# Kernel tuning notes

Hardware: AMD Instinct MI355X
Metric: run time of the kernel (lower is better)

The kernel has to match this reference:

```python
import jax, jax.numpy as jnp
import numpy as np

B, L, H = 2, 4096, 1024


def _rope_tables(seq_len, dim, base=10000.0):
    # standard RoPE cos/sin tables, rotate-half convention, shape [L, dim]
    inv_freq = 1.0 / (base ** (np.arange(0, dim, 2, dtype=np.float32) / dim))
    t = np.arange(seq_len, dtype=np.float32)
    freqs = np.outer(t, inv_freq)                      # [L, dim/2]
    emb = np.concatenate([freqs, freqs], axis=-1)      # [L, dim]
    return jnp.asarray(np.cos(emb)), jnp.asarray(np.sin(emb))


def setup_inputs() -> dict:
    key = jax.random.key(0)
    k1, k2 = jax.random.split(key)
    hidden_states = jax.random.normal(k1, (B, L, H), dtype=jnp.float32)
    # queries weight: normal with std = initializer_range / sqrt(2*num_layers*hidden)
    std = 0.02 / np.sqrt(2.0 * 24 * H)
    W_q = jax.random.normal(k2, (H, H), dtype=jnp.float32) * std
    cos, sin = _rope_tables(L, H)
    return {"hidden_states": hidden_states, "W_q": W_q, "cos": cos, "sin": sin}


def _rotate_half(x):
    x1, x2 = jnp.split(x, 2, axis=-1)
    return jnp.concatenate([-x2, x1], axis=-1)


def reference(hidden_states, W_q, cos, sin):
    # dropout with p=0.0 (eval) -> identity
    h = hidden_states * cos[None, :, :] + _rotate_half(hidden_states) * sin[None, :, :]  # RoPE, [B,L,H]
    q = jnp.einsum('blh,oh->blo', h, W_q)          # F.linear(h, W_q), [B,L,H]
    pre_attn = jnp.einsum('blh,bmh->blm', q, h)    # Q @ K^T (no softmax), [B,L,L]
    attention = jnp.einsum('blm,bmh->blh', pre_attn, h)  # scores @ V, [B,L,H]
    return attention
```

## Files before the change

### kernel.cpp

```cpp
#include <hip/hip_runtime.h>
#include <hip/hip_bf16.h>
#include <stdint.h>

#define BB 2
#define LL 4096
#define HH 1024
#define GBK 32

typedef __bf16 bf16;
typedef __bf16 bf16x4 __attribute__((ext_vector_type(4)));
typedef __bf16 bf16x8 __attribute__((ext_vector_type(8)));
typedef float  f32x4  __attribute__((ext_vector_type(4)));

__device__ __forceinline__ void async_cp16(const bf16* g, const bf16* l)
{
    typedef const uint32_t __attribute__((address_space(1)))* gp_t;
    typedef uint32_t __attribute__((address_space(3)))* lp_t;
    __builtin_amdgcn_global_load_lds((gp_t)(uintptr_t)g, (lp_t)(uintptr_t)l, 16, 0, 0);
}

__device__ __forceinline__ uint32_t pack_bf16(float lo, float hi)
{
    union { bf16 b; unsigned short u; } a, c;
    a.b = (bf16)lo; c.b = (bf16)hi;
    return (uint32_t)a.u | ((uint32_t)c.u << 16);
}

__global__ __launch_bounds__(256) void prep_kernel(
    const float* __restrict__ x, const float* __restrict__ cs,
    const float* __restrict__ sn, const float* __restrict__ Wq,
    bf16* __restrict__ h, bf16* __restrict__ hT, bf16* __restrict__ Wb)
{
    const int id = blockIdx.x;
    if (id >= 512) {
        const long base = (long)(id - 512) * 4096 + (long)threadIdx.x * 16;
#pragma unroll
        for (int j = 0; j < 4; ++j) {
            const float4 v = *(const float4*)(Wq + base + j * 4);
            bf16x4 o;
            o[0] = (bf16)v.x; o[1] = (bf16)v.y; o[2] = (bf16)v.z; o[3] = (bf16)v.w;
            *(bf16x4*)(Wb + base + j * 4) = o;
        }
        return;
    }
    __shared__ uint32_t lds[2][64][36];
    const int r0 = (id >> 3) * 64;
    const int c0 = (id & 7) * 64;
    const int t  = threadIdx.x;
    const int c8 = t & 7;
    const int rr = t >> 3;
    const int ca = c0 + c8 * 8;
    const long crow0 = (long)(r0 + 2 * rr) * HH;

    float cA[2][8], sA[2][8];
#pragma unroll
    for (int rw = 0; rw < 2; ++rw) {
        const long cr = crow0 + (long)rw * HH;
        *(float4*)&cA[rw][0] = *(const float4*)(cs + cr + ca);
        *(float4*)&cA[rw][4] = *(const float4*)(cs + cr + ca + 4);
        *(float4*)&sA[rw][0] = *(const float4*)(sn + cr + ca);
        *(float4*)&sA[rw][4] = *(const float4*)(sn + cr + ca + 4);
    }

    for (int b = 0; b < 2; ++b) {
        if (b) __syncthreads();
        float oA[2][8], oB[2][8];
#pragma unroll
        for (int rw = 0; rw < 2; ++rw) {
            const long xr = ((long)b * LL + r0 + 2 * rr + rw) * HH;
            float xA[8], xB[8];
            *(float4*)&xA[0] = *(const float4*)(x + xr + ca);
            *(float4*)&xA[4] = *(const float4*)(x + xr + ca + 4);
            *(float4*)&xB[0] = *(const float4*)(x + xr + ca + 512);
            *(float4*)&xB[4] = *(const float4*)(x + xr + ca + 516);
#pragma unroll
            for (int j = 0; j < 8; ++j) {
                oA[rw][j] = xA[j] * cA[rw][j] - xB[j] * sA[rw][j];
                oB[rw][j] = xB[j] * cA[rw][j] + xA[j] * sA[rw][j];
            }
            bf16x8 hA, hB;
#pragma unroll
            for (int j = 0; j < 8; ++j) { hA[j] = (bf16)oA[rw][j]; hB[j] = (bf16)oB[rw][j]; }
            *(bf16x8*)(h + xr + ca)       = hA;
            *(bf16x8*)(h + xr + ca + 512) = hB;
        }
#pragma unroll
        for (int j = 0; j < 8; ++j) {
            lds[0][c8 * 8 + j][rr] = pack_bf16(oA[0][j], oA[1][j]);
            lds[1][c8 * 8 + j][rr] = pack_bf16(oB[0][j], oB[1][j]);
        }
        __syncthreads();

        const int cc = t >> 2;
        const int q  = t & 3;
#pragma unroll
        for (int s = 0; s < 2; ++s) {
            const int hrow = (s ? c0 + 512 : c0) + cc;
            bf16* po = hT + (long)b * HH * LL + (long)hrow * LL + r0 + q * 16;
            const uint4 w0 = *(const uint4*)&lds[s][cc][q * 8];
            const uint4 w1 = *(const uint4*)&lds[s][cc][q * 8 + 4];
            *(uint4*)(po)     = w0;
            *(uint4*)(po + 8) = w1;
        }
    }
}

__global__ __launch_bounds__(128) void rope_kernel(
    const float* __restrict__ x, const float* __restrict__ cs,
    const float* __restrict__ sn, bf16* __restrict__ h)
{
    const int l = blockIdx.x;
    const int b = blockIdx.y;
    const int i = threadIdx.x * 4;
    const long xb = ((long)b * LL + l) * HH;
    const long cb = (long)l * HH;
    const float4 x1 = *(const float4*)(x + xb + i);
    const float4 x2 = *(const float4*)(x + xb + i + HH / 2);
    const float4 c1 = *(const float4*)(cs + cb + i);
    const float4 c2 = *(const float4*)(cs + cb + i + HH / 2);
    const float4 s1 = *(const float4*)(sn + cb + i);
    const float4 s2 = *(const float4*)(sn + cb + i + HH / 2);
    bf16x4 o1, o2;
    o1[0] = (bf16)(x1.x * c1.x - x2.x * s1.x);
    o1[1] = (bf16)(x1.y * c1.y - x2.y * s1.y);
    o1[2] = (bf16)(x1.z * c1.z - x2.z * s1.z);
    o1[3] = (bf16)(x1.w * c1.w - x2.w * s1.w);
    o2[0] = (bf16)(x2.x * c2.x + x1.x * s2.x);
    o2[1] = (bf16)(x2.y * c2.y + x1.y * s2.y);
    o2[2] = (bf16)(x2.z * c2.z + x1.z * s2.z);
    o2[3] = (bf16)(x2.w * c2.w + x1.w * s2.w);
    *(bf16x4*)(h + xb + i)          = o1;
    *(bf16x4*)(h + xb + i + HH / 2) = o2;
}

__global__ __launch_bounds__(256) void transpose_bf16_64(
    const bf16* __restrict__ in, bf16* __restrict__ out, const int R, const int C)
{
    __shared__ uint32_t lds[64][36];
    const long zoff = (long)blockIdx.z * R * C;
    const int r0 = blockIdx.x * 64;
    const int c0 = blockIdx.y * 64;
    const int t  = threadIdx.x;
    const int c8 = t & 7;
    const int rr = t >> 3;
    const bf16* p0 = in + zoff + (long)(r0 + 2 * rr) * C + c0 + c8 * 8;
    const uint4 ra = *(const uint4*)p0;
    const uint4 rb = *(const uint4*)(p0 + C);
    const uint32_t av[4] = {ra.x, ra.y, ra.z, ra.w};
    const uint32_t bv[4] = {rb.x, rb.y, rb.z, rb.w};
#pragma unroll
    for (int j = 0; j < 4; ++j) {
        const uint32_t alo = av[j] & 0xffffu, ahi = av[j] >> 16;
        const uint32_t blo = bv[j] & 0xffffu, bhi = bv[j] >> 16;
        lds[c8 * 8 + 2 * j    ][rr] = alo | (blo << 16);
        lds[c8 * 8 + 2 * j + 1][rr] = ahi | (bhi << 16);
    }
    __syncthreads();
    const int c = t >> 2;
    const int q = t & 3;
    const uint4 w0 = *(const uint4*)&lds[c][q * 8];
    const uint4 w1 = *(const uint4*)&lds[c][q * 8 + 4];
    bf16* po = out + zoff + (long)(c0 + c) * R + r0 + q * 16;
    *(uint4*)(po)     = w0;
    *(uint4*)(po + 8) = w1;
}

__global__ __launch_bounds__(256) void cast_wq(
    const float* __restrict__ Wq, bf16* __restrict__ Wb)
{
    const long idx = ((long)blockIdx.x * 256 + threadIdx.x) * 4;
    const float4 v = *(const float4*)(Wq + idx);
    bf16x4 o;
    o[0] = (bf16)v.x; o[1] = (bf16)v.y; o[2] = (bf16)v.z; o[3] = (bf16)v.w;
    *(bf16x4*)(Wb + idx) = o;
}

#define GEMM_SHARED()                                                          \
    __shared__ __align__(16) bf16 As_[2][128][32];                             \
    __shared__ __align__(16) bf16 Bs_[2][128][32];

#define GEMM_PREFETCH(KOFF, BUF)                                               \
    do {                                                                       \
        async_cp16(Ag + (KOFF),           &As_[BUF][0][0] + woff0);            \
        async_cp16(Ag + (KOFF) + 64L * K, &As_[BUF][0][0] + woff1);            \
        async_cp16(Bg + (KOFF),           &Bs_[BUF][0][0] + woff0);            \
        async_cp16(Bg + (KOFF) + 64L * K, &Bs_[BUF][0][0] + woff1);            \
    } while (0)

#define GEMM_BODY(M0, N0, KBASE, KEND, DST, DT, LDN)                           \
    {                                                                          \
        const int tid  = threadIdx.x;                                          \
        const int lane = tid & 63;                                             \
        const int wave = tid >> 6;                                             \
        const int wm = (wave & 1) * 64;                                        \
        const int wn = (wave >> 1) * 64;                                       \
        const int fr = lane & 15;                                              \
        const int fq = lane >> 4;                                              \
        const int srow = tid >> 2;                                             \
        const int scol = (tid & 3) * 8;                                        \
        const int woff0 = wave * 512;                                          \
        const int woff1 = 2048 + wave * 512;                                   \
        const bf16* Ag = Ab + (long)((M0) + srow) * K + scol;                  \
        const bf16* Bg = Bb + (long)((N0) + srow) * K + scol;                  \
        const f32x4 vzero = {0.f, 0.f, 0.f, 0.f};                              \
        f32x4 acc[4][4];                                                       \
        _Pragma("unroll") for (int i = 0; i < 4; ++i)                          \
            _Pragma("unroll") for (int j = 0; j < 4; ++j) acc[i][j] = vzero;   \
        GEMM_PREFETCH(KBASE, 0);                                               \
        int buf = 0;                                                           \
        for (int k0 = (KBASE); k0 < (KEND); k0 += GBK, buf ^= 1) {             \
            __syncthreads();                                                   \
            if (k0 + GBK < (KEND)) GEMM_PREFETCH(k0 + GBK, buf ^ 1);           \
            bf16x8 af[4], bfv[4];                                              \
            _Pragma("unroll") for (int i = 0; i < 4; ++i)                      \
                af[i]  = *(const bf16x8*)&As_[buf][wm + i * 16 + fr][fq * 8];  \
            _Pragma("unroll") for (int j = 0; j < 4; ++j)                      \
                bfv[j] = *(const bf16x8*)&Bs_[buf][wn + j * 16 + fr][fq * 8];  \
            _Pragma("unroll") for (int i = 0; i < 4; ++i)                      \
                _Pragma("unroll") for (int j = 0; j < 4; ++j)                  \
                    acc[i][j] = __builtin_amdgcn_mfma_f32_16x16x32_bf16(       \
                        af[i], bfv[j], acc[i][j], 0, 0, 0);                    \
        }                                                                      \
        _Pragma("unroll") for (int i = 0; i < 4; ++i) {                        \
            _Pragma("unroll") for (int r = 0; r < 4; ++r) {                    \
                const int row = (M0) + wm + i * 16 + fq * 4 + r;               \
                _Pragma("unroll") for (int j = 0; j < 4; ++j) {                \
                    const int col = (N0) + wn + j * 16 + fr;                   \
                    (DST)[(long)row * (LDN) + col] = (DT)acc[i][j][r];         \
                }                                                              \
            }                                                                  \
        }                                                                      \
    }

template <typename OUT_T>
__global__ __launch_bounds__(256) void gemm_bt(
    const bf16* __restrict__ A, const bf16* __restrict__ B, OUT_T* __restrict__ C,
    const int M, const int N, const int K,
    const long sA, const long sB, const long sC)
{
    GEMM_SHARED();
    const bf16* Ab = A + blockIdx.z * sA;
    const bf16* Bb = B + blockIdx.z * sB;
    OUT_T*      Cb = C + blockIdx.z * sC;
    const int m0 = blockIdx.x * 128;
    const int n0 = blockIdx.y * 128;
    GEMM_BODY(m0, n0, 0, K, Cb, OUT_T, N);
}

#define E_STAGE_A(KT, PART, BUF)                                               \
  do {                                                                         \
    const int kk0_ = kbase + (KT) * 64;                                        \
    _Pragma("unroll") for (int qq_ = 0; qq_ < 2; ++qq_) {                      \
      const int ch_  = qq_ * 512 + tid;                                        \
      const int sl_  = ch_ >> 3;                                               \
      const int cc_  = (ch_ & 7) ^ (sl_ & 7);                                  \
      const int row_ = (sl_ & 63) + (PART) * 64 + ((sl_ >> 6) << 7);           \
      async_cp16(Ab + (long)(m0 + row_) * K + kk0_ + cc_ * 8,                  \
                 &As[BUF][PART][0][0] + (qq_ * 512 + (tid & 448)) * 8);        \
    }                                                                          \
  } while (0)

#define E_STAGE_B(KT, PART, BUF)                                               \
  do {                                                                         \
    const int kk0_ = kbase + (KT) * 64;                                        \
    _Pragma("unroll") for (int qq_ = 0; qq_ < 2; ++qq_) {                      \
      const int ch_  = qq_ * 512 + tid;                                        \
      const int sl_  = ch_ >> 3;                                               \
      const int cc_  = (ch_ & 7) ^ (sl_ & 7);                                  \
      const int row_ = (sl_ & 31) + (PART) * 32 + ((sl_ >> 5) << 6);           \
      async_cp16(Bb + (long)(n0 + row_) * K + kk0_ + cc_ * 8,                  \
                 &Bs[BUF][PART][0][0] + (qq_ * 512 + (tid & 448)) * 8);        \
    }                                                                          \
  } while (0)

#define E_STAGE_B2(KT, PART, BUF)                                              \
  do {                                                                         \
    const int kk0_ = kbase + (KT) * 64;                                        \
    const int sl_  = tid >> 3;                                                 \
    const int cc_  = (tid & 7) ^ (sl_ & 7);                                    \
    const int row_ = (sl_ & 15) + (PART) * 16 + ((sl_ >> 4) << 5);             \
    async_cp16(Bb + (long)(n0 + row_) * K + kk0_ + cc_ * 8,                    \
               &Bs2[BUF][PART][0][0] + (tid & 448) * 8);                       \
  } while (0)

#define E_LOAD_A(BUF, IG)                                                      \
  do {                                                                         \
    const bf16* Ap_ = &As[BUF][IG][0][0] + (wr * 64 + fr) * 64;                \
    _Pragma("unroll") for (int ii_ = 0; ii_ < 4; ++ii_)                        \
      _Pragma("unroll") for (int kk_ = 0; kk_ < 2; ++kk_)                      \
        af[ii_][kk_] = *(const bf16x8*)(Ap_ + ii_ * 1024 +                     \
                        (((kk_ * 4 + fq) ^ fr7) * 8));                         \
  } while (0)

#define E_LOAD_Bv(BUF, JP, DSTV)                                               \
  do {                                                                         \
    const bf16* Bp_ = &Bs[BUF][JP][0][0] + (wc * 32 + fr) * 64;                \
    _Pragma("unroll") for (int jj_ = 0; jj_ < 2; ++jj_)                        \
      _Pragma("unroll") for (int kk_ = 0; kk_ < 2; ++kk_)                      \
        DSTV[jj_][kk_] = *(const bf16x8*)(Bp_ + jj_ * 1024 +                   \
                        (((kk_ * 4 + fq) ^ fr7) * 8));                         \
  } while (0)

#define E_LOAD_B2(BUF, JG, DSTV)                                               \
  do {                                                                         \
    const bf16* Bp_ = &Bs2[BUF][JG][0][0] + (wc * 16 + fr) * 64;               \
    _Pragma("unroll") for (int kk_ = 0; kk_ < 2; ++kk_)                        \
      DSTV[kk_] = *(const bf16x8*)(Bp_ + (((kk_ * 4 + fq) ^ fr7) * 8));        \
  } while (0)

#define E_MMA(IG, JG, BV)                                                      \
  do {                                                                         \
    __builtin_amdgcn_s_setprio(1);                                             \
    _Pragma("unroll") for (int ii_ = 0; ii_ < 4; ++ii_)                        \
      _Pragma("unroll") for (int jj_ = 0; jj_ < 2; ++jj_)                      \
        _Pragma("unroll") for (int kk_ = 0; kk_ < 2; ++kk_)                    \
          acc[(IG) * 4 + ii_][(JG) * 2 + jj_] =                                \
              __builtin_amdgcn_mfma_f32_16x16x32_bf16(                         \
                  af[ii_][kk_], BV[jj_][kk_],                                  \
                  acc[(IG) * 4 + ii_][(JG) * 2 + jj_], 0, 0, 0);               \
    __builtin_amdgcn_s_setprio(0);                                             \
  } while (0)

#define E_MMA2(IG, JG, BV)                                                     \
  do {                                                                         \
    __builtin_amdgcn_s_setprio(1);                                             \
    _Pragma("unroll") for (int ii_ = 0; ii_ < 4; ++ii_)                        \
      _Pragma("unroll") for (int kk_ = 0; kk_ < 2; ++kk_)                      \
        acc2[(IG) * 4 + ii_][JG] =                                             \
            __builtin_amdgcn_mfma_f32_16x16x32_bf16(                           \
                af[ii_][kk_], BV[kk_], acc2[(IG) * 4 + ii_][JG], 0, 0, 0);     \
    __builtin_amdgcn_s_setprio(0);                                             \
  } while (0)

#define E_BAR()   __builtin_amdgcn_s_barrier()
#define E_LGKM0() do { asm volatile("s_waitcnt lgkmcnt(0)" ::: "memory");      \
                       __builtin_amdgcn_sched_barrier(0); } while (0)
#define E_VM(N)   asm volatile("s_waitcnt vmcnt(" #N ")" ::: "memory")

#define E_COMMON_IDX()                                                         \
  const int tid  = threadIdx.x;                                                \
  const int lane = tid & 63;                                                   \
  const int wv   = tid >> 6;                                                   \
  const int wr   = wv >> 2;                                                    \
  const int wc   = wv & 3;                                                     \
  const int fr   = lane & 15;                                                  \
  const int fq   = lane >> 4;                                                  \
  const int fr7  = fr & 7;                                                     \
  (void)lane;

__global__ __launch_bounds__(512, 2) void gemm8_Gq(
    const bf16* __restrict__ hT, const bf16* __restrict__ Wb,
    const bf16* __restrict__ h, bf16* __restrict__ P, bf16* __restrict__ q)
{
    __shared__ __align__(16) bf16 As[2][2][128][64];
    __shared__ __align__(16) bf16 Bs[2][2][128][64];
    E_COMMON_IDX();
    bf16x8 af[4][2], bfv0[2][2], bfv1[2][2];
    f32x4 acc[8][4];
#pragma unroll
    for (int i_ = 0; i_ < 8; ++i_)
#pragma unroll
        for (int j_ = 0; j_ < 4; ++j_) acc[i_][j_] = (f32x4){0.f, 0.f, 0.f, 0.f};

    const int bid = blockIdx.x;
    const int id  = (bid & 7) * 32 + (bid >> 3);
    const bf16* Ab; const bf16* Bb;
    int K, kbase, m0, n0;
    bf16* Cb;
    if (id < 128) {
        m0 = (id >> 2) * 256;
        n0 = (id & 3) * 256;
        Ab = h; Bb = Wb; K = HH; kbase = 0;
        Cb = q;
    } else {
        const int u  = id - 128;
        const int pl = u >> 4;
        const int zb = pl >> 2;
        const int zs = pl & 3;
        const int tl = u & 15;
        m0 = (tl & 3) * 256;
        n0 = (tl >> 2) * 256;
        Ab = hT + (long)zb * HH * LL; Bb = Ab;
        K  = LL; kbase = zs * (LL / 4);
        Cb = P + (long)pl * HH * HH;
    }

    E_STAGE_A(0, 0, 0); E_STAGE_B(0, 1, 0); E_STAGE_A(0, 1, 0);
    E_STAGE_B(0, 0, 0);
    E_STAGE_A(1, 0, 1); E_STAGE_B(1, 1, 1); E_STAGE_A(1, 1, 1);
    E_VM(6); E_BAR();
    int t_ = 0;
#pragma unroll 1
    for (; t_ + 3 < 16; t_ += 2) {
         E_LOAD_A(0, 0); E_LOAD_Bv(0, 0, bfv0); E_STAGE_B(t_ + 1, 0, 1);
                 E_BAR(); E_LGKM0(); E_MMA(0, 0, bfv0); E_BAR();
         E_LOAD_Bv(0, 1, bfv1); E_STAGE_A(t_ + 2, 0, 0);
                 E_BAR(); E_LGKM0(); E_MMA(0, 1, bfv1); E_BAR();
         E_LOAD_A(0, 1); E_STAGE_B(t_ + 2, 1, 0);
                 E_BAR(); E_LGKM0(); E_MMA(1, 1, bfv1); E_BAR();
         E_STAGE_A(t_ + 2, 1, 0);
                 E_MMA(1, 0, bfv0); E_VM(6); E_BAR();
         E_LOAD_A(1, 0); E_LOAD_Bv(1, 0, bfv0); E_STAGE_B(t_ + 2, 0, 0);
                 E_BAR(); E_LGKM0(); E_MMA(0, 0, bfv0); E_BAR();
         E_LOAD_Bv(1, 1, bfv1); E_STAGE_A(t_ + 3, 0, 1);
                 E_BAR(); E_LGKM0(); E_MMA(0, 1, bfv1); E_BAR();
         E_LOAD_A(1, 1); E_STAGE_B(t_ + 3, 1, 1);
                 E_BAR(); E_LGKM0(); E_MMA(1, 1, bfv1); E_BAR();
         E_STAGE_A(t_ + 3, 1, 1);
                 E_MMA(1, 0, bfv0); E_VM(6); E_BAR();
    }
    E_LOAD_A(0, 0); E_LOAD_Bv(0, 0, bfv0); E_STAGE_B(t_ + 1, 0, 1);
    E_BAR(); E_LGKM0(); E_MMA(0, 0, bfv0); E_BAR();
    E_LOAD_Bv(0, 1, bfv1); E_BAR(); E_LGKM0(); E_MMA(0, 1, bfv1); E_BAR();
    E_LOAD_A(0, 1); E_BAR(); E_LGKM0(); E_MMA(1, 1, bfv1); E_BAR();
    E_MMA(1, 0, bfv0); E_VM(0); E_BAR();
    E_LOAD_A(1, 0); E_LOAD_Bv(1, 0, bfv0); E_BAR(); E_LGKM0(); E_MMA(0, 0, bfv0); E_BAR();
    E_LOAD_Bv(1, 1, bfv1); E_BAR(); E_LGKM0(); E_MMA(0, 1, bfv1); E_BAR();
    E_LOAD_A(1, 1); E_BAR(); E_LGKM0(); E_MMA(1, 1, bfv1); E_BAR();
    E_MMA(1, 0, bfv0);

#pragma unroll
    for (int gi = 0; gi < 8; ++gi)
#pragma unroll
        for (int r = 0; r < 4; ++r) {
            const int row = m0 + wr * 128 + gi * 16 + fq * 4 + r;
#pragma unroll
            for (int gj = 0; gj < 4; ++gj)
                Cb[(long)row * HH + n0 + wc * 64 + gj * 16 + fr] = (bf16)acc[gi][gj][r];
        }
}

__global__ __launch_bounds__(512, 2) void gemm8_qG(
    const bf16* __restrict__ qm, const bf16* __restrict__ G, float* __restrict__ out)
{
    __shared__ __align__(16) bf16 As[2][2][128][64];
    __shared__ __align__(16) bf16 Bs2[2][2][64][64];
    E_COMMON_IDX();
    bf16x8 af[4][2], bw0[2], bw1[2];
    f32x4 acc2[8][2];
#pragma unroll
    for (int i_ = 0; i_ < 8; ++i_)
#pragma unroll
        for (int j_ = 0; j_ < 2; ++j_) acc2[i_][j_] = (f32x4){0.f, 0.f, 0.f, 0.f};

    const int bid = blockIdx.x;
    const int id  = (bid & 7) * 32 + (bid >> 3);
    const int mb  = id >> 3;
    const int b   = mb >> 4;
    const int m0  = (mb & 15) * 256;
    const int n0  = (id & 7) * 128;
    const bf16* Ab = qm + (long)b * LL * HH;
    const bf16* Bb = G + (long)b * HH * HH;
    const int K = HH, kbase = 0;
    float* outb = out + (long)b * LL * HH;

    E_STAGE_A(0, 0, 0); E_STAGE_B2(0, 1, 0); E_STAGE_A(0, 1, 0);
    E_STAGE_B2(0, 0, 0);
    E_STAGE_A(1, 0, 1); E_STAGE_B2(1, 1, 1); E_STAGE_A(1, 1, 1);
    E_VM(5); E_BAR();
    int t_ = 0;
#pragma unroll 1
    for (; t_ + 3 < 16; t_ += 2) {
         E_LOAD_A(0, 0); E_LOAD_B2(0, 0, bw0); E_STAGE_B2(t_ + 1, 0, 1);
                 E_BAR(); E_LGKM0(); E_MMA2(0, 0, bw0); E_BAR();
         E_LOAD_B2(0, 1, bw1); E_STAGE_A(t_ + 2, 0, 0);
                 E_BAR(); E_LGKM0(); E_MMA2(0, 1, bw1); E_BAR();
         E_LOAD_A(0, 1); E_STAGE_B2(t_ + 2, 1, 0);
                 E_BAR(); E_LGKM0(); E_MMA2(1, 1, bw1); E_BAR();
         E_STAGE_A(t_ + 2, 1, 0);
                 E_MMA2(1, 0, bw0); E_VM(5); E_BAR();
         E_LOAD_A(1, 0); E_LOAD_B2(1, 0, bw0); E_STAGE_B2(t_ + 2, 0, 0);
                 E_BAR(); E_LGKM0(); E_MMA2(0, 0, bw0); E_BAR();
         E_LOAD_B2(1, 1, bw1); E_STAGE_A(t_ + 3, 0, 1);
                 E_BAR(); E_LGKM0(); E_MMA2(0, 1, bw1); E_BAR();
         E_LOAD_A(1, 1); E_STAGE_B2(t_ + 3, 1, 1);
                 E_BAR(); E_LGKM0(); E_MMA2(1, 1, bw1); E_BAR();
         E_STAGE_A(t_ + 3, 1, 1);
                 E_MMA2(1, 0, bw0); E_VM(5); E_BAR();
    }
    E_LOAD_A(0, 0); E_LOAD_B2(0, 0, bw0); E_STAGE_B2(t_ + 1, 0, 1);
    E_BAR(); E_LGKM0(); E_MMA2(0, 0, bw0); E_BAR();
    E_LOAD_B2(0, 1, bw1); E_BAR(); E_LGKM0(); E_MMA2(0, 1, bw1); E_BAR();
    E_LOAD_A(0, 1); E_BAR(); E_LGKM0(); E_MMA2(1, 1, bw1); E_BAR();
    E_MMA2(1, 0, bw0); E_VM(0); E_BAR();
    E_LOAD_A(1, 0); E_LOAD_B2(1, 0, bw0); E_BAR(); E_LGKM0(); E_MMA2(0, 0, bw0); E_BAR();
    E_LOAD_B2(1, 1, bw1); E_BAR(); E_LGKM0(); E_MMA2(0, 1, bw1); E_BAR();
    E_LOAD_A(1, 1); E_BAR(); E_LGKM0(); E_MMA2(1, 1, bw1); E_BAR();
    E_MMA2(1, 0, bw0);

#pragma unroll
    for (int gi = 0; gi < 8; ++gi)
#pragma unroll
        for (int r = 0; r < 4; ++r) {
            const int row = m0 + wr * 128 + gi * 16 + fq * 4 + r;
#pragma unroll
            for (int gj = 0; gj < 2; ++gj)
                outb[(long)row * HH + n0 + wc * 32 + gj * 16 + fr] = acc2[gi][gj][r];
        }
}

__global__ __launch_bounds__(256) void reduce_splits(
    const bf16* __restrict__ P, bf16* __restrict__ out, const int npb, const int S)
{
    const int b = blockIdx.y;
    const long r = ((long)blockIdx.x * 256 + threadIdx.x) * 8;
    const bf16* base = P + (long)b * S * npb + r;
    float a[8];
    {
        const bf16x8 v = *(const bf16x8*)(base);
#pragma unroll
        for (int j = 0; j < 8; ++j) a[j] = (float)v[j];
    }
    for (int s = 1; s < S; ++s) {
        const bf16x8 v = *(const bf16x8*)(base + (long)s * npb);
#pragma unroll
        for (int j = 0; j < 8; ++j) a[j] += (float)v[j];
    }
    bf16x8 o;
#pragma unroll
    for (int j = 0; j < 8; ++j) o[j] = (bf16)a[j];
    *(bf16x8*)(out + (long)b * npb + r) = o;
}

extern "C" void kernel_launch(void* const* d_in, const int* in_sizes, int n_in,
                              void* d_out, int out_size, void* d_ws, size_t ws_size,
                              hipStream_t stream)
{
    const float* x  = (const float*)d_in[0];
    const float* Wq = (const float*)d_in[1];
    const float* cs = (const float*)d_in[2];
    const float* sn = (const float*)d_in[3];
    float* out = (float*)d_out;
    char* ws = (char*)d_ws;

    bf16*  h  = (bf16*)(ws);
    bf16*  hT = (bf16*)(ws + 16u * 1024 * 1024);
    bf16*  Wb = (bf16*)(ws + 32u * 1024 * 1024);
    bf16*  G  = (bf16*)(ws + 34u * 1024 * 1024);
    bf16*  P  = (bf16*)(ws + 38u * 1024 * 1024);

    const bool big_ws = ws_size >= (size_t)90 * 1024 * 1024;
    bf16* q = big_ws ? (bf16*)(ws + 70u * 1024 * 1024)
                     : (bf16*)(ws + 54u * 1024 * 1024);

    if (big_ws) {
        prep_kernel<<<dim3(768), 256, 0, stream>>>(x, cs, sn, Wq, h, hT, Wb);
        gemm8_Gq<<<dim3(256), 512, 0, stream>>>(hT, Wb, h, P, q);
        reduce_splits<<<dim3(HH * HH / 2048, BB), 256, 0, stream>>>(P, G, HH * HH, 4);
        gemm8_qG<<<dim3(256), 512, 0, stream>>>(q, G, out);
    } else {
        rope_kernel<<<dim3(LL, BB), 128, 0, stream>>>(x, cs, sn, h);
        transpose_bf16_64<<<dim3(LL / 64, HH / 64, BB), 256, 0, stream>>>(h, hT, LL, HH);
        cast_wq<<<dim3(HH * HH / 1024), 256, 0, stream>>>(Wq, Wb);
        gemm_bt<bf16><<<dim3(HH / 128, HH / 128, BB), 256, 0, stream>>>(
            hT, hT, G, HH, HH, LL, (long)HH * LL, (long)HH * LL, (long)HH * HH);
        gemm_bt<bf16><<<dim3(LL / 128, HH / 128, BB), 256, 0, stream>>>(
            h, Wb, q, LL, HH, HH, (long)LL * HH, 0L, (long)LL * HH);
        gemm_bt<float><<<dim3(LL / 128, HH / 128, BB), 256, 0, stream>>>(
            q, G, out, LL, HH, HH, (long)LL * HH, (long)HH * HH, (long)LL * HH);
    }
}
```

Baseline: 167.7 us.

## Reassociate matmuls to form Wq·G once instead of projecting all queries

Exploits associativity: the per-token query projection q = h·Wqᵀ is no longer computed. Instead a small per-batch 1024×1024 matrix M = G·Wq is formed and used directly as the right-hand operand of the final GEMM (out = h·Mᵀ, relying on G being symmetric). This cuts the large L×H×H projection GEMM and replaces it with an H×H×H split-K GEMM plus an extra reduction. The prep kernel now transposes Wq while casting it, and the G GEMM is re-split into 8 K-chunks so it still fills 256 blocks. The cost is two extra kernel launches on the critical path and an extra bf16 rounding of M.

```diff
diff --git a/kernel.cpp b/kernel.cpp
--- a/kernel.cpp
+++ b/kernel.cpp
@@ -29,24 +29,39 @@
 __global__ __launch_bounds__(256) void prep_kernel(
     const float* __restrict__ x, const float* __restrict__ cs,
     const float* __restrict__ sn, const float* __restrict__ Wq,
-    bf16* __restrict__ h, bf16* __restrict__ hT, bf16* __restrict__ Wb)
+    bf16* __restrict__ h, bf16* __restrict__ hT, bf16* __restrict__ WqT)
 {
     const int id = blockIdx.x;
+    const int t  = threadIdx.x;
     if (id >= 512) {
-        const long base = (long)(id - 512) * 4096 + (long)threadIdx.x * 16;
-#pragma unroll
-        for (int j = 0; j < 4; ++j) {
-            const float4 v = *(const float4*)(Wq + base + j * 4);
-            bf16x4 o;
-            o[0] = (bf16)v.x; o[1] = (bf16)v.y; o[2] = (bf16)v.z; o[3] = (bf16)v.w;
-            *(bf16x4*)(Wb + base + j * 4) = o;
-        }
+        __shared__ uint32_t tl[64][36];
+        const int id2 = id - 512;
+        const int tr0 = (id2 >> 4) * 64;
+        const int tc0 = (id2 & 15) * 64;
+        const int c8 = t & 7;
+        const int rr = t >> 3;
+        const float* p0 = Wq + (long)(tr0 + 2 * rr) * HH + tc0 + c8 * 8;
+        float ra[8], rb[8];
+        *(float4*)&ra[0] = *(const float4*)(p0);
+        *(float4*)&ra[4] = *(const float4*)(p0 + 4);
+        *(float4*)&rb[0] = *(const float4*)(p0 + HH);
+        *(float4*)&rb[4] = *(const float4*)(p0 + HH + 4);
+#pragma unroll
+        for (int j = 0; j < 8; ++j)
+            tl[c8 * 8 + j][rr] = pack_bf16(ra[j], rb[j]);
+        __syncthreads();
+        const int cc = t >> 2;
+        const int qq = t & 3;
+        bf16* po = WqT + (long)(tc0 + cc) * HH + tr0 + qq * 16;
+        const uint4 w0 = *(const uint4*)&tl[cc][qq * 8];
+        const uint4 w1 = *(const uint4*)&tl[cc][qq * 8 + 4];
+        *(uint4*)(po)     = w0;
+        *(uint4*)(po + 8) = w1;
         return;
     }
     __shared__ uint32_t lds[2][64][36];
     const int r0 = (id >> 3) * 64;
     const int c0 = (id & 7) * 64;
-    const int t  = threadIdx.x;
     const int c8 = t & 7;
     const int rr = t >> 3;
     const int ca = c0 + c8 * 8;
@@ -247,6 +262,25 @@
     GEMM_BODY(m0, n0, 0, K, Cb, OUT_T, N);
 }
 
+__global__ __launch_bounds__(256) void gemm_mt(
+    const bf16* __restrict__ G, const bf16* __restrict__ WqT, bf16* __restrict__ Pm)
+{
+    GEMM_SHARED();
+    const int id = blockIdx.x;
+    const int b  = id >> 8;
+    const int rs = id & 255;
+    const int s  = rs >> 6;
+    const int tl = rs & 63;
+    const int m0 = (tl & 7) * 128;
+    const int n0 = (tl >> 3) * 128;
+    const bf16* Ab = G + (long)b * HH * HH;
+    const bf16* Bb = WqT;
+    bf16* Cb = Pm + (long)(b * 4 + s) * HH * HH;
+    const int K = HH;
+    const int kbase = s * 256;
+    GEMM_BODY(m0, n0, kbase, kbase + 256, Cb, bf16, HH);
+}
+
 #define E_STAGE_A(KT, PART, BUF)                                               \
   do {                                                                         \
     const int kk0_ = kbase + (KT) * 64;                                        \
@@ -348,9 +382,8 @@
   const int fr7  = fr & 7;                                                     \
   (void)lane;
 
-__global__ __launch_bounds__(512, 2) void gemm8_Gq(
-    const bf16* __restrict__ hT, const bf16* __restrict__ Wb,
-    const bf16* __restrict__ h, bf16* __restrict__ P, bf16* __restrict__ q)
+__global__ __launch_bounds__(512, 2) void gemm8_G(
+    const bf16* __restrict__ hT, bf16* __restrict__ P)
 {
     __shared__ __align__(16) bf16 As[2][2][128][64];
     __shared__ __align__(16) bf16 Bs[2][2][128][64];
@@ -364,26 +397,17 @@
 
     const int bid = blockIdx.x;
     const int id  = (bid & 7) * 32 + (bid >> 3);
-    const bf16* Ab; const bf16* Bb;
-    int K, kbase, m0, n0;
-    bf16* Cb;
-    if (id < 128) {
-        m0 = (id >> 2) * 256;
-        n0 = (id & 3) * 256;
-        Ab = h; Bb = Wb; K = HH; kbase = 0;
-        Cb = q;
-    } else {
-        const int u  = id - 128;
-        const int pl = u >> 4;
-        const int zb = pl >> 2;
-        const int zs = pl & 3;
-        const int tl = u & 15;
-        m0 = (tl & 3) * 256;
-        n0 = (tl >> 2) * 256;
-        Ab = hT + (long)zb * HH * LL; Bb = Ab;
-        K  = LL; kbase = zs * (LL / 4);
-        Cb = P + (long)pl * HH * HH;
-    }
+    const int pl  = id >> 4;
+    const int zb  = pl >> 3;
+    const int zs  = pl & 7;
+    const int tl  = id & 15;
+    const int m0  = (tl & 3) * 256;
+    const int n0  = (tl >> 2) * 256;
+    const bf16* Ab = hT + (long)zb * HH * LL;
+    const bf16* Bb = Ab;
+    const int K = LL;
+    const int kbase = zs * (LL / 8);
+    bf16* Cb = P + (long)pl * HH * HH;
 
     E_STAGE_A(0, 0, 0); E_STAGE_B(0, 1, 0); E_STAGE_A(0, 1, 0);
     E_STAGE_B(0, 0, 0);
@@ -391,7 +415,7 @@
     E_VM(6); E_BAR();
     int t_ = 0;
 #pragma unroll 1
-    for (; t_ + 3 < 16; t_ += 2) {
+    for (; t_ + 3 < 8; t_ += 2) {
          E_LOAD_A(0, 0); E_LOAD_Bv(0, 0, bfv0); E_STAGE_B(t_ + 1, 0, 1);
                  E_BAR(); E_LGKM0(); E_MMA(0, 0, bfv0); E_BAR();
          E_LOAD_Bv(0, 1, bfv1); E_STAGE_A(t_ + 2, 0, 0);
@@ -533,22 +557,26 @@
     float* out = (float*)d_out;
     char* ws = (char*)d_ws;
 
-    bf16*  h  = (bf16*)(ws);
-    bf16*  hT = (bf16*)(ws + 16u * 1024 * 1024);
-    bf16*  Wb = (bf16*)(ws + 32u * 1024 * 1024);
-    bf16*  G  = (bf16*)(ws + 34u * 1024 * 1024);
-    bf16*  P  = (bf16*)(ws + 38u * 1024 * 1024);
+    bf16*  h   = (bf16*)(ws);
+    bf16*  hT  = (bf16*)(ws + 16u * 1024 * 1024);
+    bf16*  WqT = (bf16*)(ws + 32u * 1024 * 1024);
+    bf16*  G   = (bf16*)(ws + 34u * 1024 * 1024);
+    bf16*  P   = (bf16*)(ws + 38u * 1024 * 1024);
+    bf16*  Pm  = P;
+    bf16*  Mt  = (bf16*)(ws + 70u * 1024 * 1024);
 
     const bool big_ws = ws_size >= (size_t)90 * 1024 * 1024;
-    bf16* q = big_ws ? (bf16*)(ws + 70u * 1024 * 1024)
-                     : (bf16*)(ws + 54u * 1024 * 1024);
 
     if (big_ws) {
-        prep_kernel<<<dim3(768), 256, 0, stream>>>(x, cs, sn, Wq, h, hT, Wb);
-        gemm8_Gq<<<dim3(256), 512, 0, stream>>>(hT, Wb, h, P, q);
-        reduce_splits<<<dim3(HH * HH / 2048, BB), 256, 0, stream>>>(P, G, HH * HH, 4);
-        gemm8_qG<<<dim3(256), 512, 0, stream>>>(q, G, out);
+        prep_kernel<<<dim3(768), 256, 0, stream>>>(x, cs, sn, Wq, h, hT, WqT);
+        gemm8_G<<<dim3(256), 512, 0, stream>>>(hT, P);
+        reduce_splits<<<dim3(HH * HH / 2048, BB), 256, 0, stream>>>(P, G, HH * HH, 8);
+        gemm_mt<<<dim3(512), 256, 0, stream>>>(G, WqT, Pm);
+        reduce_splits<<<dim3(HH * HH / 2048, BB), 256, 0, stream>>>(Pm, Mt, HH * HH, 4);
+        gemm8_qG<<<dim3(256), 512, 0, stream>>>(h, Mt, out);
     } else {
+        bf16* Wb = WqT;
+        bf16* q  = (bf16*)(ws + 54u * 1024 * 1024);
         rope_kernel<<<dim3(LL, BB), 128, 0, stream>>>(x, cs, sn, h);
         transpose_bf16_64<<<dim3(LL / 64, HH / 64, BB), 256, 0, stream>>>(h, hT, LL, HH);
         cast_wq<<<dim3(HH * HH / 1024), 256, 0, stream>>>(Wq, Wb);
```

Result: slower. 176.3 us (+5.1%).
